# Optimization experiments

Hardware: AMD Instinct MI355X
Metric: run time of the kernel (lower is better)

The kernel has to match this reference:

```python
import jax, jax.numpy as jnp
import numpy as np

N_NODES = 100000
NEG_SLOPE = 0.01


def setup_inputs() -> dict:
    key = jax.random.key(0)
    k1, k2, k3, k4 = jax.random.split(key, 4)
    E = 1600000
    x = jax.random.normal(k1, (N_NODES, 256), dtype=jnp.float32)
    edge_index = jax.random.randint(k2, (2, E), 0, N_NODES, dtype=jnp.int64)
    # Glorot-ish init for GCN linear weights
    W1 = jax.random.normal(k3, (256, 128), dtype=jnp.float32) / np.sqrt(256.0)
    b1 = jnp.zeros((128,), dtype=jnp.float32)
    W2 = jax.random.normal(k4, (128, 64), dtype=jnp.float32) / np.sqrt(128.0)
    b2 = jnp.zeros((64,), dtype=jnp.float32)
    return {"x": x, "edge_index": edge_index, "W1": W1, "b1": b1, "W2": W2, "b2": b2}


def _gcn_norm(edge_index, n_nodes):
    # Add self-loops (PyG GCNConv default), symmetric normalization.
    loops = jnp.arange(n_nodes, dtype=edge_index.dtype)
    src = jnp.concatenate([edge_index[0], loops])
    dst = jnp.concatenate([edge_index[1], loops])
    deg = jax.ops.segment_sum(jnp.ones_like(dst, dtype=jnp.float32), dst,
                              num_segments=n_nodes)
    dinv = jnp.where(deg > 0, 1.0 / jnp.sqrt(deg), 0.0)
    norm = dinv[src] * dinv[dst]  # [E + N]
    return src, dst, norm


def _gcn_conv(h, W, b, src, dst, norm, n_nodes):
    h = h @ W                              # [N, out] linear transform first
    msg = h[src] * norm[:, None]           # gather + edge weighting
    agg = jax.ops.segment_sum(msg, dst, num_segments=n_nodes)  # scatter-add
    return agg + b


def reference(x, edge_index, W1, b1, W2, b2):
    n = x.shape[0]
    src, dst, norm = _gcn_norm(edge_index, n)
    h = _gcn_conv(x, W1, b1, src, dst, norm, n)
    h = jnp.where(h >= 0, h, NEG_SLOPE * h)  # leaky_relu, slope 0.01
    return _gcn_conv(h, W2, b2, src, dst, norm, n)
```

## Files before the change

kernel.cpp:

```cpp
#include <hip/hip_runtime.h>
#include <hip/hip_bf16.h>
#include <stdint.h>

#define GPART 512
#define BSHIFT 9
#define BSIZE 512
#define MAXNB 512

typedef short short8 __attribute__((ext_vector_type(8)));
typedef float f32x4 __attribute__((ext_vector_type(4)));
union U4S8 { uint4 u; short8 s; };

static __device__ __forceinline__ float bflo(uint32_t h){ return __uint_as_float(h << 16); }
static __device__ __forceinline__ float bfhi(uint32_t h){ return __uint_as_float(h & 0xFFFF0000u); }
static __device__ __forceinline__ uint32_t f2bf_bits(float f){
  uint32_t u = __float_as_uint(f);
  return (u + 0x7FFFu + ((u >> 16) & 1u)) >> 16;
}
static __device__ __forceinline__ uint32_t pack2bf(float lo, float hi){
  return f2bf_bits(lo) | (f2bf_bits(hi) << 16);
}

__global__ __launch_bounds__(256) void k_hist(const int* __restrict__ dst, int E, int NB,
    int* __restrict__ gHist){
  __shared__ int lh[MAXNB];
  int blk = blockIdx.x;
  for (int i = threadIdx.x; i < NB; i += 256) lh[i] = 0;
  __syncthreads();
  int chunk = (E + GPART - 1) / GPART;
  int e0 = blk * chunk, e1 = min(E, e0 + chunk);
  for (int e = e0 + threadIdx.x; e < e1; e += 256)
    atomicAdd(&lh[dst[e] >> BSHIFT], 1);
  __syncthreads();
  for (int i = threadIdx.x; i < NB; i += 256) gHist[i * GPART + blk] = lh[i];
}

__global__ __launch_bounds__(64) void k_scanA(int* __restrict__ gHist,
    int* __restrict__ bucketTotal){
  int b = blockIdx.x;
  int lane = threadIdx.x;
  int carry = 0;
  #pragma unroll
  for (int r = 0; r < GPART/64; ++r){
    int v = gHist[b*GPART + r*64 + lane];
    int pref = v;
    #pragma unroll
    for (int off = 1; off < 64; off <<= 1){ int t = __shfl_up(pref, off); if (lane >= off) pref += t; }
    int tot = __shfl(pref, 63);
    gHist[b*GPART + r*64 + lane] = carry + pref - v;
    carry += tot;
  }
  if (lane == 0) bucketTotal[b] = carry;
}

__global__ __launch_bounds__(64) void k_scanB(const int* __restrict__ bucketTotal, int NB,
    int* __restrict__ bucketBase){
  int lane = threadIdx.x;
  int carry = 0;
  for (int r = 0; r*64 < NB; ++r){
    int idx = r*64 + lane;
    int v = (idx < NB) ? bucketTotal[idx] : 0;
    int pref = v;
    #pragma unroll
    for (int off = 1; off < 64; off <<= 1){ int t = __shfl_up(pref, off); if (lane >= off) pref += t; }
    int tot = __shfl(pref, 63);
    if (idx < NB) bucketBase[idx] = carry + pref - v;
    carry += tot;
  }
}

__global__ __launch_bounds__(256) void k_scatter(const int* __restrict__ src,
    const int* __restrict__ dst, int E, int NB,
    const int* __restrict__ gHist, const int* __restrict__ bucketBase,
    uint32_t* __restrict__ edgesP){
  __shared__ int lpos[MAXNB];
  int blk = blockIdx.x;
  for (int i = threadIdx.x; i < NB; i += 256) lpos[i] = 0;
  __syncthreads();
  int chunk = (E + GPART - 1) / GPART;
  int e0 = blk * chunk, e1 = min(E, e0 + chunk);
  for (int e = e0 + threadIdx.x; e < e1; e += 256){
    int s = src[e], d = dst[e];
    int b = d >> BSHIFT;
    int o = atomicAdd(&lpos[b], 1);
    int pos = bucketBase[b] + gHist[b*GPART + blk] + o;
    edgesP[pos] = (uint32_t)s | ((uint32_t)(d & (BSIZE-1)) << 23);
  }
}

__global__ __launch_bounds__(256) void k_csr_p1(const uint32_t* __restrict__ edgesP,
    const int* __restrict__ bucketBase, const int* __restrict__ bucketTotal,
    int n, int* __restrict__ start, int* __restrict__ cnt, float* __restrict__ dinv){
  __shared__ int cnt_l[BSIZE], start_l[BSIZE];
  int b = blockIdx.x;
  int base = bucketBase[b], total = bucketTotal[b];
  int d0 = b << BSHIFT;
  int tid = threadIdx.x;
  for (int i = tid; i < BSIZE; i += 256) cnt_l[i] = 0;
  __syncthreads();
  for (int i = tid; i < total; i += 256)
    atomicAdd(&cnt_l[edgesP[base + i] >> 23], 1);
  __syncthreads();
  if (tid < 64){
    int lane = tid, carry = 0;
    #pragma unroll
    for (int r = 0; r < BSIZE/64; ++r){
      int v = cnt_l[r*64 + lane];
      int pref = v;
      #pragma unroll
      for (int off = 1; off < 64; off <<= 1){ int t = __shfl_up(pref, off); if (lane >= off) pref += t; }
      int tot = __shfl(pref, 63);
      start_l[r*64 + lane] = carry + pref - v;
      carry += tot;
    }
  }
  __syncthreads();
  for (int i = tid; i < BSIZE; i += 256){
    int d = d0 + i;
    if (d < n){
      int c = cnt_l[i];
      cnt[d] = c;
      start[d] = base + start_l[i];
      dinv[d] = rsqrtf((float)(c + 1));
    }
  }
}

__global__ __launch_bounds__(256) void k_csr_p2(const uint32_t* __restrict__ edgesP,
    const int* __restrict__ bucketBase, const int* __restrict__ bucketTotal,
    const int* __restrict__ start, const float* __restrict__ dinv,
    int2* __restrict__ csr){
  __shared__ int fp[BSIZE];
  int b = blockIdx.x;
  int base = bucketBase[b], total = bucketTotal[b];
  int d0 = b << BSHIFT;
  int tid = threadIdx.x;
  for (int i = tid; i < BSIZE; i += 256) fp[i] = 0;
  __syncthreads();
  for (int i = tid; i < total; i += 256){
    uint32_t w = edgesP[base + i];
    int dl = (int)(w >> 23);
    int s = (int)(w & 0x7FFFFFu);
    int p = atomicAdd(&fp[dl], 1);
    float wt = dinv[s] * dinv[d0 + dl];
    csr[start[d0 + dl] + p] = make_int2(s, __float_as_int(wt));
  }
}

__global__ __launch_bounds__(256) void k_packW(const float* __restrict__ W,
    uint4* __restrict__ Wf, int K, int Nc){
  int s = blockIdx.x * 256 + threadIdx.x;
  int total = (K >> 5) * (Nc >> 4) * 64;
  if (s >= total) return;
  int lane = s & 63;
  int frag = s >> 6;
  int NT = Nc >> 4;
  int nt = frag % NT, ks = frag / NT;
  int col = nt*16 + (lane & 15);
  int k0  = ks*32 + (lane >> 4)*8;
  float v[8];
  #pragma unroll
  for (int e = 0; e < 8; ++e) v[e] = W[(size_t)(k0 + e)*Nc + col];
  uint4 u;
  u.x = pack2bf(v[0], v[1]); u.y = pack2bf(v[2], v[3]);
  u.z = pack2bf(v[4], v[5]); u.w = pack2bf(v[6], v[7]);
  Wf[s] = u;
}

__global__ __launch_bounds__(256) void k_gemm1_mfma(const float* __restrict__ X,
    const uint4* __restrict__ W1f, unsigned short* __restrict__ H1, int n){
  int wv = (int)((blockIdx.x * 256u + threadIdx.x) >> 6);
  int lane = threadIdx.x & 63;
  int row0 = wv * 16;
  if (row0 >= n) return;
  int rA = lane & 15, kg = lane >> 4;
  f32x4 acc[8];
  #pragma unroll
  for (int nt = 0; nt < 8; ++nt) acc[nt] = (f32x4){0.f, 0.f, 0.f, 0.f};
  int r0 = min(row0 + rA, n - 1);
  const float* x0 = X + (size_t)r0*256 + kg*8;
  float4 fa = *(const float4*)(x0);
  float4 fb = *(const float4*)(x0 + 4);
  for (int ks = 0; ks < 8; ++ks){
    U4S8 a;
    a.u.x = pack2bf(fa.x, fa.y); a.u.y = pack2bf(fa.z, fa.w);
    a.u.z = pack2bf(fb.x, fb.y); a.u.w = pack2bf(fb.z, fb.w);
    if (ks < 7){
      fa = *(const float4*)(x0 + (ks+1)*32);
      fb = *(const float4*)(x0 + (ks+1)*32 + 4);
    }
    #pragma unroll
    for (int nt = 0; nt < 8; ++nt){
      U4S8 b; b.u = W1f[(ks*8 + nt)*64 + lane];
      acc[nt] = __builtin_amdgcn_mfma_f32_16x16x32_bf16(a.s, b.s, acc[nt], 0, 0, 0);
    }
  }
  #pragma unroll
  for (int r = 0; r < 4; ++r){
    int row = row0 + kg*4 + r;
    if (row < n){
      #pragma unroll
      for (int nt = 0; nt < 8; ++nt)
        H1[(size_t)row*128 + nt*16 + rA] = (unsigned short)f2bf_bits(acc[nt][r]);
    }
  }
}

__global__ __launch_bounds__(256) void k_agg1(const uint4* __restrict__ H1,
    const int2* __restrict__ csr,
    const int* __restrict__ start, const int* __restrict__ cnt,
    const float* __restrict__ dinv, const float* __restrict__ b1,
    uint4* __restrict__ A1, int n){
  int w = (int)((blockIdx.x * blockDim.x + threadIdx.x) >> 6);
  int lane = threadIdx.x & 63;
  if (w >= n) return;
  int g = lane >> 4, li = lane & 15;
  float dw = dinv[w];
  float sw = (g == 0) ? dw * dw : 0.f;
  uint4 hs = H1[(size_t)w*16 + li];
  float acc[8];
  acc[0]=sw*bflo(hs.x); acc[1]=sw*bfhi(hs.x); acc[2]=sw*bflo(hs.y); acc[3]=sw*bfhi(hs.y);
  acc[4]=sw*bflo(hs.z); acc[5]=sw*bfhi(hs.z); acc[6]=sw*bflo(hs.w); acc[7]=sw*bfhi(hs.w);
  int e0 = start[w], deg = cnt[w];
  for (int base = 0; base < deg; base += 64){
    int nin = min(64, deg - base);
    int2 ew = (lane < nin) ? csr[e0 + base + lane] : make_int2(0, 0);
    for (int j = 0; j < nin; j += 8){
      int   sA = __shfl(ew.x, j + g);
      float wA = __uint_as_float((uint32_t)__shfl(ew.y, j + g));
      int   sB = __shfl(ew.x, j + 4 + g);
      float wB = __uint_as_float((uint32_t)__shfl(ew.y, j + 4 + g));
      uint4 hA = H1[(size_t)sA*16 + li];
      uint4 hB = H1[(size_t)sB*16 + li];
      acc[0]=fmaf(wA,bflo(hA.x),acc[0]); acc[1]=fmaf(wA,bfhi(hA.x),acc[1]);
      acc[2]=fmaf(wA,bflo(hA.y),acc[2]); acc[3]=fmaf(wA,bfhi(hA.y),acc[3]);
      acc[4]=fmaf(wA,bflo(hA.z),acc[4]); acc[5]=fmaf(wA,bfhi(hA.z),acc[5]);
      acc[6]=fmaf(wA,bflo(hA.w),acc[6]); acc[7]=fmaf(wA,bfhi(hA.w),acc[7]);
      acc[0]=fmaf(wB,bflo(hB.x),acc[0]); acc[1]=fmaf(wB,bfhi(hB.x),acc[1]);
      acc[2]=fmaf(wB,bflo(hB.y),acc[2]); acc[3]=fmaf(wB,bfhi(hB.y),acc[3]);
      acc[4]=fmaf(wB,bflo(hB.z),acc[4]); acc[5]=fmaf(wB,bfhi(hB.z),acc[5]);
      acc[6]=fmaf(wB,bflo(hB.w),acc[6]); acc[7]=fmaf(wB,bfhi(hB.w),acc[7]);
    }
  }
  #pragma unroll
  for (int e = 0; e < 8; ++e){
    acc[e] += __shfl_xor(acc[e], 16);
    acc[e] += __shfl_xor(acc[e], 32);
  }
  float4 bA = *(const float4*)&b1[li*8];
  float4 bB = *(const float4*)&b1[li*8 + 4];
  acc[0]+=bA.x; acc[1]+=bA.y; acc[2]+=bA.z; acc[3]+=bA.w;
  acc[4]+=bB.x; acc[5]+=bB.y; acc[6]+=bB.z; acc[7]+=bB.w;
  #pragma unroll
  for (int e = 0; e < 8; ++e) acc[e] = (acc[e] >= 0.f) ? acc[e] : 0.01f * acc[e];
  if (g == 0){
    uint4 o;
    o.x = pack2bf(acc[0], acc[1]); o.y = pack2bf(acc[2], acc[3]);
    o.z = pack2bf(acc[4], acc[5]); o.w = pack2bf(acc[6], acc[7]);
    A1[(size_t)w*16 + li] = o;
  }
}

__global__ __launch_bounds__(256) void k_gemm2_mfma(const uint4* __restrict__ A1,
    const uint4* __restrict__ W2f, unsigned short* __restrict__ H2, int n){
  int wv = (int)((blockIdx.x * 256u + threadIdx.x) >> 6);
  int lane = threadIdx.x & 63;
  int row0 = wv * 16;
  if (row0 >= n) return;
  int rA = lane & 15, kg = lane >> 4;
  f32x4 acc[4];
  #pragma unroll
  for (int nt = 0; nt < 4; ++nt) acc[nt] = (f32x4){0.f, 0.f, 0.f, 0.f};
  int r0 = min(row0 + rA, n - 1);
  const uint4* arow = A1 + (size_t)r0*16 + kg;
  uint4 u = arow[0];
  #pragma unroll
  for (int ks = 0; ks < 4; ++ks){
    U4S8 a; a.u = u;
    if (ks < 3) u = arow[(ks+1)*4];
    #pragma unroll
    for (int nt = 0; nt < 4; ++nt){
      U4S8 b; b.u = W2f[(ks*4 + nt)*64 + lane];
      acc[nt] = __builtin_amdgcn_mfma_f32_16x16x32_bf16(a.s, b.s, acc[nt], 0, 0, 0);
    }
  }
  #pragma unroll
  for (int r = 0; r < 4; ++r){
    int row = row0 + kg*4 + r;
    if (row < n){
      #pragma unroll
      for (int nt = 0; nt < 4; ++nt)
        H2[(size_t)row*64 + nt*16 + rA] = (unsigned short)f2bf_bits(acc[nt][r]);
    }
  }
}

__global__ __launch_bounds__(256) void k_agg2(const uint4* __restrict__ H2,
    const int2* __restrict__ csr,
    const int* __restrict__ start, const int* __restrict__ cnt,
    const float* __restrict__ dinv, const float* __restrict__ b2,
    float* __restrict__ out, int n){
  int w = (int)((blockIdx.x * blockDim.x + threadIdx.x) >> 6);
  int lane = threadIdx.x & 63;
  if (w >= n) return;
  int g = lane >> 3, li = lane & 7;
  float dw = dinv[w];
  float sw = (g == 0) ? dw * dw : 0.f;
  uint4 hs = H2[(size_t)w*8 + li];
  float acc[8];
  acc[0]=sw*bflo(hs.x); acc[1]=sw*bfhi(hs.x); acc[2]=sw*bflo(hs.y); acc[3]=sw*bfhi(hs.y);
  acc[4]=sw*bflo(hs.z); acc[5]=sw*bfhi(hs.z); acc[6]=sw*bflo(hs.w); acc[7]=sw*bfhi(hs.w);
  int e0 = start[w], deg = cnt[w];
  for (int base = 0; base < deg; base += 64){
    int nin = min(64, deg - base);
    int2 ew = (lane < nin) ? csr[e0 + base + lane] : make_int2(0, 0);
    for (int j = 0; j < nin; j += 16){
      int   sA = __shfl(ew.x, j + g);
      float wA = __uint_as_float((uint32_t)__shfl(ew.y, j + g));
      int   sB = __shfl(ew.x, j + 8 + g);
      float wB = __uint_as_float((uint32_t)__shfl(ew.y, j + 8 + g));
      uint4 hA = H2[(size_t)sA*8 + li];
      uint4 hB = H2[(size_t)sB*8 + li];
      acc[0]=fmaf(wA,bflo(hA.x),acc[0]); acc[1]=fmaf(wA,bfhi(hA.x),acc[1]);
      acc[2]=fmaf(wA,bflo(hA.y),acc[2]); acc[3]=fmaf(wA,bfhi(hA.y),acc[3]);
      acc[4]=fmaf(wA,bflo(hA.z),acc[4]); acc[5]=fmaf(wA,bfhi(hA.z),acc[5]);
      acc[6]=fmaf(wA,bflo(hA.w),acc[6]); acc[7]=fmaf(wA,bfhi(hA.w),acc[7]);
      acc[0]=fmaf(wB,bflo(hB.x),acc[0]); acc[1]=fmaf(wB,bfhi(hB.x),acc[1]);
      acc[2]=fmaf(wB,bflo(hB.y),acc[2]); acc[3]=fmaf(wB,bfhi(hB.y),acc[3]);
      acc[4]=fmaf(wB,bflo(hB.z),acc[4]); acc[5]=fmaf(wB,bfhi(hB.z),acc[5]);
      acc[6]=fmaf(wB,bflo(hB.w),acc[6]); acc[7]=fmaf(wB,bfhi(hB.w),acc[7]);
    }
  }
  #pragma unroll
  for (int e = 0; e < 8; ++e){
    acc[e] += __shfl_xor(acc[e], 8);
    acc[e] += __shfl_xor(acc[e], 16);
    acc[e] += __shfl_xor(acc[e], 32);
  }
  float4 bA = *(const float4*)&b2[li*8];
  float4 bB = *(const float4*)&b2[li*8 + 4];
  acc[0]+=bA.x; acc[1]+=bA.y; acc[2]+=bA.z; acc[3]+=bA.w;
  acc[4]+=bB.x; acc[5]+=bB.y; acc[6]+=bB.z; acc[7]+=bB.w;
  if (g == 0){
    float4 o0 = make_float4(acc[0], acc[1], acc[2], acc[3]);
    float4 o1 = make_float4(acc[4], acc[5], acc[6], acc[7]);
    *(float4*)&out[(size_t)w*64 + li*8]     = o0;
    *(float4*)&out[(size_t)w*64 + li*8 + 4] = o1;
  }
}

extern "C" void kernel_launch(void* const* d_in, const int* in_sizes, int n_in,
                              void* d_out, int out_size, void* d_ws, size_t ws_size,
                              hipStream_t stream){
  const float* x  = (const float*)d_in[0];
  const int*   ei = (const int*)d_in[1];
  const float* W1 = (const float*)d_in[2];
  const float* b1 = (const float*)d_in[3];
  const float* W2 = (const float*)d_in[4];
  const float* b2 = (const float*)d_in[5];
  float* out = (float*)d_out;

  int N = in_sizes[0] / 256;
  int E = in_sizes[1] / 2;
  int NB = (N + BSIZE - 1) >> BSHIFT;

  char* p = (char*)d_ws;
  uint32_t* H1   = (uint32_t*)p;  p += (size_t)N*64*4;
  uint32_t* A1   = (uint32_t*)p;  p += (size_t)N*64*4;
  uint32_t* H2   = (uint32_t*)p;  p += (size_t)N*32*4;
  uint32_t* edgesP=(uint32_t*)p;  p += (size_t)E*4;
  int2* csr      = (int2*)p;      p += (size_t)E*8;
  int* gHist     = (int*)p;       p += (size_t)NB*GPART*4;
  int* bucketTotal=(int*)p;       p += (size_t)((NB+63)&~63)*4;
  int* bucketBase= (int*)p;       p += (size_t)((NB+63)&~63)*4;
  uint4* W1f     = (uint4*)p;     p += 8*8*64*16;
  uint4* W2f     = (uint4*)p;     p += 4*4*64*16;
  int* start     = (int*)p;       p += (size_t)N*4;
  int* cnt       = (int*)p;       p += (size_t)N*4;
  float* dinv    = (float*)p;     p += (size_t)N*4;

  const int* srcIdx = ei;
  const int* dstIdx = ei + E;

  int nW = (N + 15) / 16;
  int nWaveBlocks = (nW + 3) / 4;

  k_packW<<<(8*8*64 + 255)/256, 256, 0, stream>>>(W1, W1f, 256, 128);
  k_packW<<<(4*4*64 + 255)/256, 256, 0, stream>>>(W2, W2f, 128, 64);
  k_hist<<<GPART, 256, 0, stream>>>(dstIdx, E, NB, gHist);
  k_scanA<<<NB, 64, 0, stream>>>(gHist, bucketTotal);
  k_scanB<<<1, 64, 0, stream>>>(bucketTotal, NB, bucketBase);
  k_scatter<<<GPART, 256, 0, stream>>>(srcIdx, dstIdx, E, NB, gHist, bucketBase, edgesP);
  k_csr_p1<<<NB, 256, 0, stream>>>(edgesP, bucketBase, bucketTotal, N, start, cnt, dinv);
  k_csr_p2<<<NB, 256, 0, stream>>>(edgesP, bucketBase, bucketTotal, start, dinv, csr);
  k_gemm1_mfma<<<nWaveBlocks, 256, 0, stream>>>(x, W1f, (unsigned short*)H1, N);
  k_agg1<<<(N+3)/4, 256, 0, stream>>>((const uint4*)H1, csr, start, cnt, dinv, b1, (uint4*)A1, N);
  k_gemm2_mfma<<<nWaveBlocks, 256, 0, stream>>>((const uint4*)A1, W2f, (unsigned short*)H2, N);
  k_agg2<<<(N+3)/4, 256, 0, stream>>>((const uint4*)H2, csr, start, cnt, dinv, b2, out, N);
}
```

Baseline: 216.4 us.

## Use nontemporal loads/stores for streaming data and prefetch gathers in aggregation

```diff
diff --git a/kernel.cpp b/kernel.cpp
--- a/kernel.cpp
+++ b/kernel.cpp
@@ -9,6 +9,9 @@
 
 typedef short short8 __attribute__((ext_vector_type(8)));
 typedef float f32x4 __attribute__((ext_vector_type(4)));
+typedef uint32_t u32x4 __attribute__((ext_vector_type(4)));
+typedef uint32_t u32x2 __attribute__((ext_vector_type(2)));
+typedef float f32x4v __attribute__((ext_vector_type(4)));
 union U4S8 { uint4 u; short8 s; };
 
 static __device__ __forceinline__ float bflo(uint32_t h){ return __uint_as_float(h << 16); }
@@ -30,7 +33,7 @@
   int chunk = (E + GPART - 1) / GPART;
   int e0 = blk * chunk, e1 = min(E, e0 + chunk);
   for (int e = e0 + threadIdx.x; e < e1; e += 256)
-    atomicAdd(&lh[dst[e] >> BSHIFT], 1);
+    atomicAdd(&lh[__builtin_nontemporal_load(&dst[e]) >> BSHIFT], 1);
   __syncthreads();
   for (int i = threadIdx.x; i < NB; i += 256) gHist[i * GPART + blk] = lh[i];
 }
@@ -80,11 +83,13 @@
   int chunk = (E + GPART - 1) / GPART;
   int e0 = blk * chunk, e1 = min(E, e0 + chunk);
   for (int e = e0 + threadIdx.x; e < e1; e += 256){
-    int s = src[e], d = dst[e];
+    int s = __builtin_nontemporal_load(&src[e]);
+    int d = __builtin_nontemporal_load(&dst[e]);
     int b = d >> BSHIFT;
     int o = atomicAdd(&lpos[b], 1);
     int pos = bucketBase[b] + gHist[b*GPART + blk] + o;
-    edgesP[pos] = (uint32_t)s | ((uint32_t)(d & (BSIZE-1)) << 23);
+    uint32_t v = (uint32_t)s | ((uint32_t)(d & (BSIZE-1)) << 23);
+    __builtin_nontemporal_store(v, &edgesP[pos]);
   }
 }
 
@@ -99,7 +104,7 @@
   for (int i = tid; i < BSIZE; i += 256) cnt_l[i] = 0;
   __syncthreads();
   for (int i = tid; i < total; i += 256)
-    atomicAdd(&cnt_l[edgesP[base + i] >> 23], 1);
+    atomicAdd(&cnt_l[__builtin_nontemporal_load(&edgesP[base + i]) >> 23], 1);
   __syncthreads();
   if (tid < 64){
     int lane = tid, carry = 0;
@@ -138,12 +143,13 @@
   for (int i = tid; i < BSIZE; i += 256) fp[i] = 0;
   __syncthreads();
   for (int i = tid; i < total; i += 256){
-    uint32_t w = edgesP[base + i];
+    uint32_t w = __builtin_nontemporal_load(&edgesP[base + i]);
     int dl = (int)(w >> 23);
     int s = (int)(w & 0x7FFFFFu);
     int p = atomicAdd(&fp[dl], 1);
     float wt = dinv[s] * dinv[d0 + dl];
-    csr[start[d0 + dl] + p] = make_int2(s, __float_as_int(wt));
+    u32x2 v; v.x = (uint32_t)s; v.y = __float_as_uint(wt);
+    __builtin_nontemporal_store(v, (u32x2*)&csr[start[d0 + dl] + p]);
   }
 }
 
@@ -179,15 +185,15 @@
   for (int nt = 0; nt < 8; ++nt) acc[nt] = (f32x4){0.f, 0.f, 0.f, 0.f};
   int r0 = min(row0 + rA, n - 1);
   const float* x0 = X + (size_t)r0*256 + kg*8;
-  float4 fa = *(const float4*)(x0);
-  float4 fb = *(const float4*)(x0 + 4);
+  f32x4v fa = __builtin_nontemporal_load((const f32x4v*)(x0));
+  f32x4v fb = __builtin_nontemporal_load((const f32x4v*)(x0 + 4));
   for (int ks = 0; ks < 8; ++ks){
     U4S8 a;
-    a.u.x = pack2bf(fa.x, fa.y); a.u.y = pack2bf(fa.z, fa.w);
-    a.u.z = pack2bf(fb.x, fb.y); a.u.w = pack2bf(fb.z, fb.w);
+    a.u.x = pack2bf(fa[0], fa[1]); a.u.y = pack2bf(fa[2], fa[3]);
+    a.u.z = pack2bf(fb[0], fb[1]); a.u.w = pack2bf(fb[2], fb[3]);
     if (ks < 7){
-      fa = *(const float4*)(x0 + (ks+1)*32);
-      fb = *(const float4*)(x0 + (ks+1)*32 + 4);
+      fa = __builtin_nontemporal_load((const f32x4v*)(x0 + (ks+1)*32));
+      fb = __builtin_nontemporal_load((const f32x4v*)(x0 + (ks+1)*32 + 4));
     }
     #pragma unroll
     for (int nt = 0; nt < 8; ++nt){
@@ -224,14 +230,29 @@
   int e0 = start[w], deg = cnt[w];
   for (int base = 0; base < deg; base += 64){
     int nin = min(64, deg - base);
-    int2 ew = (lane < nin) ? csr[e0 + base + lane] : make_int2(0, 0);
-    for (int j = 0; j < nin; j += 8){
-      int   sA = __shfl(ew.x, j + g);
-      float wA = __uint_as_float((uint32_t)__shfl(ew.y, j + g));
-      int   sB = __shfl(ew.x, j + 4 + g);
-      float wB = __uint_as_float((uint32_t)__shfl(ew.y, j + 4 + g));
-      uint4 hA = H1[(size_t)sA*16 + li];
-      uint4 hB = H1[(size_t)sB*16 + li];
+    int2 ew;
+    if (lane < nin){
+      u32x2 t = __builtin_nontemporal_load((const u32x2*)&csr[e0 + base + lane]);
+      ew.x = (int)t.x; ew.y = (int)t.y;
+    } else { ew = make_int2(0, 0); }
+    int ninp = (nin + 7) & ~7;
+    int   sA = __shfl(ew.x, g);
+    int   sB = __shfl(ew.x, 4 + g);
+    float wA = __uint_as_float((uint32_t)__shfl(ew.y, g));
+    float wB = __uint_as_float((uint32_t)__shfl(ew.y, 4 + g));
+    uint4 hA = H1[(size_t)sA*16 + li];
+    uint4 hB = H1[(size_t)sB*16 + li];
+    for (int j = 0; j < ninp; j += 8){
+      uint4 hA2, hB2; float wA2 = 0.f, wB2 = 0.f;
+      int jn = j + 8;
+      if (jn < ninp){
+        int sA2 = __shfl(ew.x, jn + g);
+        int sB2 = __shfl(ew.x, jn + 4 + g);
+        wA2 = __uint_as_float((uint32_t)__shfl(ew.y, jn + g));
+        wB2 = __uint_as_float((uint32_t)__shfl(ew.y, jn + 4 + g));
+        hA2 = H1[(size_t)sA2*16 + li];
+        hB2 = H1[(size_t)sB2*16 + li];
+      }
       acc[0]=fmaf(wA,bflo(hA.x),acc[0]); acc[1]=fmaf(wA,bfhi(hA.x),acc[1]);
       acc[2]=fmaf(wA,bflo(hA.y),acc[2]); acc[3]=fmaf(wA,bfhi(hA.y),acc[3]);
       acc[4]=fmaf(wA,bflo(hA.z),acc[4]); acc[5]=fmaf(wA,bfhi(hA.z),acc[5]);
@@ -240,6 +261,7 @@
       acc[2]=fmaf(wB,bflo(hB.y),acc[2]); acc[3]=fmaf(wB,bfhi(hB.y),acc[3]);
       acc[4]=fmaf(wB,bflo(hB.z),acc[4]); acc[5]=fmaf(wB,bfhi(hB.z),acc[5]);
       acc[6]=fmaf(wB,bflo(hB.w),acc[6]); acc[7]=fmaf(wB,bfhi(hB.w),acc[7]);
+      hA = hA2; hB = hB2; wA = wA2; wB = wB2;
     }
   }
   #pragma unroll
@@ -254,10 +276,10 @@
   #pragma unroll
   for (int e = 0; e < 8; ++e) acc[e] = (acc[e] >= 0.f) ? acc[e] : 0.01f * acc[e];
   if (g == 0){
-    uint4 o;
+    u32x4 o;
     o.x = pack2bf(acc[0], acc[1]); o.y = pack2bf(acc[2], acc[3]);
     o.z = pack2bf(acc[4], acc[5]); o.w = pack2bf(acc[6], acc[7]);
-    A1[(size_t)w*16 + li] = o;
+    __builtin_nontemporal_store(o, (u32x4*)&A1[(size_t)w*16 + li]);
   }
 }
 
@@ -272,12 +294,12 @@
   #pragma unroll
   for (int nt = 0; nt < 4; ++nt) acc[nt] = (f32x4){0.f, 0.f, 0.f, 0.f};
   int r0 = min(row0 + rA, n - 1);
-  const uint4* arow = A1 + (size_t)r0*16 + kg;
-  uint4 u = arow[0];
+  const u32x4* arow = (const u32x4*)(A1 + (size_t)r0*16 + kg);
+  u32x4 u = __builtin_nontemporal_load(arow);
   #pragma unroll
   for (int ks = 0; ks < 4; ++ks){
-    U4S8 a; a.u = u;
-    if (ks < 3) u = arow[(ks+1)*4];
+    U4S8 a; a.u.x = u.x; a.u.y = u.y; a.u.z = u.z; a.u.w = u.w;
+    if (ks < 3) u = __builtin_nontemporal_load(arow + (ks+1)*4);
     #pragma unroll
     for (int nt = 0; nt < 4; ++nt){
       U4S8 b; b.u = W2f[(ks*4 + nt)*64 + lane];
@@ -313,14 +335,29 @@
   int e0 = start[w], deg = cnt[w];
   for (int base = 0; base < deg; base += 64){
     int nin = min(64, deg - base);
-    int2 ew = (lane < nin) ? csr[e0 + base + lane] : make_int2(0, 0);
-    for (int j = 0; j < nin; j += 16){
-      int   sA = __shfl(ew.x, j + g);
-      float wA = __uint_as_float((uint32_t)__shfl(ew.y, j + g));
-      int   sB = __shfl(ew.x, j + 8 + g);
-      float wB = __uint_as_float((uint32_t)__shfl(ew.y, j + 8 + g));
-      uint4 hA = H2[(size_t)sA*8 + li];
-      uint4 hB = H2[(size_t)sB*8 + li];
+    int2 ew;
+    if (lane < nin){
+      u32x2 t = __builtin_nontemporal_load((const u32x2*)&csr[e0 + base + lane]);
+      ew.x = (int)t.x; ew.y = (int)t.y;
+    } else { ew = make_int2(0, 0); }
+    int ninp = (nin + 15) & ~15;
+    int   sA = __shfl(ew.x, g);
+    int   sB = __shfl(ew.x, 8 + g);
+    float wA = __uint_as_float((uint32_t)__shfl(ew.y, g));
+    float wB = __uint_as_float((uint32_t)__shfl(ew.y, 8 + g));
+    uint4 hA = H2[(size_t)sA*8 + li];
+    uint4 hB = H2[(size_t)sB*8 + li];
+    for (int j = 0; j < ninp; j += 16){
+      uint4 hA2, hB2; float wA2 = 0.f, wB2 = 0.f;
+      int jn = j + 16;
+      if (jn < ninp){
+        int sA2 = __shfl(ew.x, jn + g);
+        int sB2 = __shfl(ew.x, jn + 8 + g);
+        wA2 = __uint_as_float((uint32_t)__shfl(ew.y, jn + g));
+        wB2 = __uint_as_float((uint32_t)__shfl(ew.y, jn + 8 + g));
+        hA2 = H2[(size_t)sA2*8 + li];
+        hB2 = H2[(size_t)sB2*8 + li];
+      }
       acc[0]=fmaf(wA,bflo(hA.x),acc[0]); acc[1]=fmaf(wA,bfhi(hA.x),acc[1]);
       acc[2]=fmaf(wA,bflo(hA.y),acc[2]); acc[3]=fmaf(wA,bfhi(hA.y),acc[3]);
       acc[4]=fmaf(wA,bflo(hA.z),acc[4]); acc[5]=fmaf(wA,bfhi(hA.z),acc[5]);
@@ -329,6 +366,7 @@
       acc[2]=fmaf(wB,bflo(hB.y),acc[2]); acc[3]=fmaf(wB,bfhi(hB.y),acc[3]);
       acc[4]=fmaf(wB,bflo(hB.z),acc[4]); acc[5]=fmaf(wB,bfhi(hB.z),acc[5]);
       acc[6]=fmaf(wB,bflo(hB.w),acc[6]); acc[7]=fmaf(wB,bfhi(hB.w),acc[7]);
+      hA = hA2; hB = hB2; wA = wA2; wB = wB2;
     }
   }
   #pragma unroll
@@ -342,10 +380,10 @@
   acc[0]+=bA.x; acc[1]+=bA.y; acc[2]+=bA.z; acc[3]+=bA.w;
   acc[4]+=bB.x; acc[5]+=bB.y; acc[6]+=bB.z; acc[7]+=bB.w;
   if (g == 0){
-    float4 o0 = make_float4(acc[0], acc[1], acc[2], acc[3]);
-    float4 o1 = make_float4(acc[4], acc[5], acc[6], acc[7]);
-    *(float4*)&out[(size_t)w*64 + li*8]     = o0;
-    *(float4*)&out[(size_t)w*64 + li*8 + 4] = o1;
+    f32x4v o0; o0[0]=acc[0]; o0[1]=acc[1]; o0[2]=acc[2]; o0[3]=acc[3];
+    f32x4v o1; o1[0]=acc[4]; o1[1]=acc[5]; o1[2]=acc[6]; o1[3]=acc[7];
+    __builtin_nontemporal_store(o0, (f32x4v*)&out[(size_t)w*64 + li*8]);
+    __builtin_nontemporal_store(o1, (f32x4v*)&out[(size_t)w*64 + li*8 + 4]);
   }
 }
 
```

New measurement: 308.7 us. 42.7% more time.

## Split layer-1 aggregation into two column-half passes and software-pipeline gathers

Applied to the files above, without the earlier changes.

```diff
diff --git a/kernel.cpp b/kernel.cpp
--- a/kernel.cpp
+++ b/kernel.cpp
@@ -168,7 +168,8 @@
 }
 
 __global__ __launch_bounds__(256) void k_gemm1_mfma(const float* __restrict__ X,
-    const uint4* __restrict__ W1f, unsigned short* __restrict__ H1, int n){
+    const uint4* __restrict__ W1f, unsigned short* __restrict__ H1a,
+    unsigned short* __restrict__ H1b, int n){
   int wv = (int)((blockIdx.x * 256u + threadIdx.x) >> 6);
   int lane = threadIdx.x & 63;
   int row0 = wv * 16;
@@ -200,68 +201,76 @@
     int row = row0 + kg*4 + r;
     if (row < n){
       #pragma unroll
-      for (int nt = 0; nt < 8; ++nt)
-        H1[(size_t)row*128 + nt*16 + rA] = (unsigned short)f2bf_bits(acc[nt][r]);
-    }
-  }
-}
-
-__global__ __launch_bounds__(256) void k_agg1(const uint4* __restrict__ H1,
+      for (int nt = 0; nt < 4; ++nt)
+        H1a[(size_t)row*64 + nt*16 + rA] = (unsigned short)f2bf_bits(acc[nt][r]);
+      #pragma unroll
+      for (int nt = 4; nt < 8; ++nt)
+        H1b[(size_t)row*64 + (nt-4)*16 + rA] = (unsigned short)f2bf_bits(acc[nt][r]);
+    }
+  }
+}
+
+__global__ __launch_bounds__(256) void k_agg1_pass(const uint2* __restrict__ H1p,
     const int2* __restrict__ csr,
     const int* __restrict__ start, const int* __restrict__ cnt,
-    const float* __restrict__ dinv, const float* __restrict__ b1,
-    uint4* __restrict__ A1, int n){
+    const float* __restrict__ dinv, const float* __restrict__ b1p,
+    uint2* __restrict__ A1p, int n){
   int w = (int)((blockIdx.x * blockDim.x + threadIdx.x) >> 6);
   int lane = threadIdx.x & 63;
   if (w >= n) return;
   int g = lane >> 4, li = lane & 15;
   float dw = dinv[w];
   float sw = (g == 0) ? dw * dw : 0.f;
-  uint4 hs = H1[(size_t)w*16 + li];
-  float acc[8];
+  uint2 hs = H1p[(size_t)w*16 + li];
+  float acc[4];
   acc[0]=sw*bflo(hs.x); acc[1]=sw*bfhi(hs.x); acc[2]=sw*bflo(hs.y); acc[3]=sw*bfhi(hs.y);
-  acc[4]=sw*bflo(hs.z); acc[5]=sw*bfhi(hs.z); acc[6]=sw*bflo(hs.w); acc[7]=sw*bfhi(hs.w);
   int e0 = start[w], deg = cnt[w];
   for (int base = 0; base < deg; base += 64){
     int nin = min(64, deg - base);
     int2 ew = (lane < nin) ? csr[e0 + base + lane] : make_int2(0, 0);
-    for (int j = 0; j < nin; j += 8){
-      int   sA = __shfl(ew.x, j + g);
-      float wA = __uint_as_float((uint32_t)__shfl(ew.y, j + g));
-      int   sB = __shfl(ew.x, j + 4 + g);
-      float wB = __uint_as_float((uint32_t)__shfl(ew.y, j + 4 + g));
-      uint4 hA = H1[(size_t)sA*16 + li];
-      uint4 hB = H1[(size_t)sB*16 + li];
+    int ninp = (nin + 7) & ~7;
+    int   sA = __shfl(ew.x, g);
+    int   sB = __shfl(ew.x, 4 + g);
+    float wA = __uint_as_float((uint32_t)__shfl(ew.y, g));
+    float wB = __uint_as_float((uint32_t)__shfl(ew.y, 4 + g));
+    uint2 hA = H1p[(size_t)sA*16 + li];
+    uint2 hB = H1p[(size_t)sB*16 + li];
+    for (int j = 0; j < ninp; j += 8){
+      uint2 hA2 = hA, hB2 = hB; float wA2 = 0.f, wB2 = 0.f;
+      int jn = j + 8;
+      if (jn < ninp){
+        int sA2 = __shfl(ew.x, jn + g);
+        int sB2 = __shfl(ew.x, jn + 4 + g);
+        wA2 = __uint_as_float((uint32_t)__shfl(ew.y, jn + g));
+        wB2 = __uint_as_float((uint32_t)__shfl(ew.y, jn + 4 + g));
+        hA2 = H1p[(size_t)sA2*16 + li];
+        hB2 = H1p[(size_t)sB2*16 + li];
+      }
       acc[0]=fmaf(wA,bflo(hA.x),acc[0]); acc[1]=fmaf(wA,bfhi(hA.x),acc[1]);
       acc[2]=fmaf(wA,bflo(hA.y),acc[2]); acc[3]=fmaf(wA,bfhi(hA.y),acc[3]);
-      acc[4]=fmaf(wA,bflo(hA.z),acc[4]); acc[5]=fmaf(wA,bfhi(hA.z),acc[5]);
-      acc[6]=fmaf(wA,bflo(hA.w),acc[6]); acc[7]=fmaf(wA,bfhi(hA.w),acc[7]);
       acc[0]=fmaf(wB,bflo(hB.x),acc[0]); acc[1]=fmaf(wB,bfhi(hB.x),acc[1]);
       acc[2]=fmaf(wB,bflo(hB.y),acc[2]); acc[3]=fmaf(wB,bfhi(hB.y),acc[3]);
-      acc[4]=fmaf(wB,bflo(hB.z),acc[4]); acc[5]=fmaf(wB,bfhi(hB.z),acc[5]);
-      acc[6]=fmaf(wB,bflo(hB.w),acc[6]); acc[7]=fmaf(wB,bfhi(hB.w),acc[7]);
-    }
-  }
-  #pragma unroll
-  for (int e = 0; e < 8; ++e){
+      hA = hA2; hB = hB2; wA = wA2; wB = wB2;
+    }
+  }
+  #pragma unroll
+  for (int e = 0; e < 4; ++e){
     acc[e] += __shfl_xor(acc[e], 16);
     acc[e] += __shfl_xor(acc[e], 32);
   }
-  float4 bA = *(const float4*)&b1[li*8];
-  float4 bB = *(const float4*)&b1[li*8 + 4];
-  acc[0]+=bA.x; acc[1]+=bA.y; acc[2]+=bA.z; acc[3]+=bA.w;
-  acc[4]+=bB.x; acc[5]+=bB.y; acc[6]+=bB.z; acc[7]+=bB.w;
-  #pragma unroll
-  for (int e = 0; e < 8; ++e) acc[e] = (acc[e] >= 0.f) ? acc[e] : 0.01f * acc[e];
+  float4 bb = *(const float4*)&b1p[li*4];
+  acc[0]+=bb.x; acc[1]+=bb.y; acc[2]+=bb.z; acc[3]+=bb.w;
+  #pragma unroll
+  for (int e = 0; e < 4; ++e) acc[e] = (acc[e] >= 0.f) ? acc[e] : 0.01f * acc[e];
   if (g == 0){
-    uint4 o;
+    uint2 o;
     o.x = pack2bf(acc[0], acc[1]); o.y = pack2bf(acc[2], acc[3]);
-    o.z = pack2bf(acc[4], acc[5]); o.w = pack2bf(acc[6], acc[7]);
-    A1[(size_t)w*16 + li] = o;
-  }
-}
-
-__global__ __launch_bounds__(256) void k_gemm2_mfma(const uint4* __restrict__ A1,
+    A1p[(size_t)w*16 + li] = o;
+  }
+}
+
+__global__ __launch_bounds__(256) void k_gemm2_mfma(const uint4* __restrict__ A1a,
+    const uint4* __restrict__ A1b,
     const uint4* __restrict__ W2f, unsigned short* __restrict__ H2, int n){
   int wv = (int)((blockIdx.x * 256u + threadIdx.x) >> 6);
   int lane = threadIdx.x & 63;
@@ -272,12 +281,15 @@
   #pragma unroll
   for (int nt = 0; nt < 4; ++nt) acc[nt] = (f32x4){0.f, 0.f, 0.f, 0.f};
   int r0 = min(row0 + rA, n - 1);
-  const uint4* arow = A1 + (size_t)r0*16 + kg;
-  uint4 u = arow[0];
+  const uint4* rowa = A1a + (size_t)r0*8 + kg;
+  const uint4* rowb = A1b + (size_t)r0*8 + kg;
+  uint4 u = rowa[0];
   #pragma unroll
   for (int ks = 0; ks < 4; ++ks){
     U4S8 a; a.u = u;
-    if (ks < 3) u = arow[(ks+1)*4];
+    if (ks == 0) u = rowa[4];
+    else if (ks == 1) u = rowb[0];
+    else if (ks == 2) u = rowb[4];
     #pragma unroll
     for (int nt = 0; nt < 4; ++nt){
       U4S8 b; b.u = W2f[(ks*4 + nt)*64 + lane];
@@ -314,13 +326,24 @@
   for (int base = 0; base < deg; base += 64){
     int nin = min(64, deg - base);
     int2 ew = (lane < nin) ? csr[e0 + base + lane] : make_int2(0, 0);
-    for (int j = 0; j < nin; j += 16){
-      int   sA = __shfl(ew.x, j + g);
-      float wA = __uint_as_float((uint32_t)__shfl(ew.y, j + g));
-      int   sB = __shfl(ew.x, j + 8 + g);
-      float wB = __uint_as_float((uint32_t)__shfl(ew.y, j + 8 + g));
-      uint4 hA = H2[(size_t)sA*8 + li];
-      uint4 hB = H2[(size_t)sB*8 + li];
+    int ninp = (nin + 15) & ~15;
+    int   sA = __shfl(ew.x, g);
+    int   sB = __shfl(ew.x, 8 + g);
+    float wA = __uint_as_float((uint32_t)__shfl(ew.y, g));
+    float wB = __uint_as_float((uint32_t)__shfl(ew.y, 8 + g));
+    uint4 hA = H2[(size_t)sA*8 + li];
+    uint4 hB = H2[(size_t)sB*8 + li];
+    for (int j = 0; j < ninp; j += 16){
+      uint4 hA2 = hA, hB2 = hB; float wA2 = 0.f, wB2 = 0.f;
+      int jn = j + 16;
+      if (jn < ninp){
+        int sA2 = __shfl(ew.x, jn + g);
+        int sB2 = __shfl(ew.x, jn + 8 + g);
+        wA2 = __uint_as_float((uint32_t)__shfl(ew.y, jn + g));
+        wB2 = __uint_as_float((uint32_t)__shfl(ew.y, jn + 8 + g));
+        hA2 = H2[(size_t)sA2*8 + li];
+        hB2 = H2[(size_t)sB2*8 + li];
+      }
       acc[0]=fmaf(wA,bflo(hA.x),acc[0]); acc[1]=fmaf(wA,bfhi(hA.x),acc[1]);
       acc[2]=fmaf(wA,bflo(hA.y),acc[2]); acc[3]=fmaf(wA,bfhi(hA.y),acc[3]);
       acc[4]=fmaf(wA,bflo(hA.z),acc[4]); acc[5]=fmaf(wA,bfhi(hA.z),acc[5]);
@@ -329,6 +352,7 @@
       acc[2]=fmaf(wB,bflo(hB.y),acc[2]); acc[3]=fmaf(wB,bfhi(hB.y),acc[3]);
       acc[4]=fmaf(wB,bflo(hB.z),acc[4]); acc[5]=fmaf(wB,bfhi(hB.z),acc[5]);
       acc[6]=fmaf(wB,bflo(hB.w),acc[6]); acc[7]=fmaf(wB,bfhi(hB.w),acc[7]);
+      hA = hA2; hB = hB2; wA = wA2; wB = wB2;
     }
   }
   #pragma unroll
@@ -365,8 +389,10 @@
   int NB = (N + BSIZE - 1) >> BSHIFT;
 
   char* p = (char*)d_ws;
-  uint32_t* H1   = (uint32_t*)p;  p += (size_t)N*64*4;
-  uint32_t* A1   = (uint32_t*)p;  p += (size_t)N*64*4;
+  uint32_t* H1a  = (uint32_t*)p;  p += (size_t)N*32*4;
+  uint32_t* H1b  = (uint32_t*)p;  p += (size_t)N*32*4;
+  uint32_t* A1a  = (uint32_t*)p;  p += (size_t)N*32*4;
+  uint32_t* A1b  = (uint32_t*)p;  p += (size_t)N*32*4;
   uint32_t* H2   = (uint32_t*)p;  p += (size_t)N*32*4;
   uint32_t* edgesP=(uint32_t*)p;  p += (size_t)E*4;
   int2* csr      = (int2*)p;      p += (size_t)E*8;
@@ -384,6 +410,7 @@
 
   int nW = (N + 15) / 16;
   int nWaveBlocks = (nW + 3) / 4;
+  int nNodeBlocks = (N + 3) / 4;
 
   k_packW<<<(8*8*64 + 255)/256, 256, 0, stream>>>(W1, W1f, 256, 128);
   k_packW<<<(4*4*64 + 255)/256, 256, 0, stream>>>(W2, W2f, 128, 64);
@@ -393,8 +420,13 @@
   k_scatter<<<GPART, 256, 0, stream>>>(srcIdx, dstIdx, E, NB, gHist, bucketBase, edgesP);
   k_csr_p1<<<NB, 256, 0, stream>>>(edgesP, bucketBase, bucketTotal, N, start, cnt, dinv);
   k_csr_p2<<<NB, 256, 0, stream>>>(edgesP, bucketBase, bucketTotal, start, dinv, csr);
-  k_gemm1_mfma<<<nWaveBlocks, 256, 0, stream>>>(x, W1f, (unsigned short*)H1, N);
-  k_agg1<<<(N+3)/4, 256, 0, stream>>>((const uint4*)H1, csr, start, cnt, dinv, b1, (uint4*)A1, N);
-  k_gemm2_mfma<<<nWaveBlocks, 256, 0, stream>>>((const uint4*)A1, W2f, (unsigned short*)H2, N);
-  k_agg2<<<(N+3)/4, 256, 0, stream>>>((const uint4*)H2, csr, start, cnt, dinv, b2, out, N);
-}
+  k_gemm1_mfma<<<nWaveBlocks, 256, 0, stream>>>(x, W1f,
+      (unsigned short*)H1a, (unsigned short*)H1b, N);
+  k_agg1_pass<<<nNodeBlocks, 256, 0, stream>>>((const uint2*)H1a, csr, start, cnt,
+      dinv, b1,      (uint2*)A1a, N);
+  k_agg1_pass<<<nNodeBlocks, 256, 0, stream>>>((const uint2*)H1b, csr, start, cnt,
+      dinv, b1 + 64, (uint2*)A1b, N);
+  k_gemm2_mfma<<<nWaveBlocks, 256, 0, stream>>>((const uint4*)A1a, (const uint4*)A1b,
+      W2f, (unsigned short*)H2, N);
+  k_agg2<<<nNodeBlocks, 256, 0, stream>>>((const uint4*)H2, csr, start, cnt, dinv, b2, out, N);
+}
```

Result: slower. 245.7 us (+13.6%).

## Stage X tiles in LDS via async global_load_lds for first GEMM

Applied to the files above, without the earlier changes.

```diff
diff --git a/kernel.cpp b/kernel.cpp
--- a/kernel.cpp
+++ b/kernel.cpp
@@ -167,41 +167,51 @@
   Wf[s] = u;
 }
 
-__global__ __launch_bounds__(256) void k_gemm1_mfma(const float* __restrict__ X,
+__global__ __launch_bounds__(256) void k_gemm1_lds(const float* __restrict__ X,
     const uint4* __restrict__ W1f, unsigned short* __restrict__ H1, int n){
-  int wv = (int)((blockIdx.x * 256u + threadIdx.x) >> 6);
-  int lane = threadIdx.x & 63;
-  int row0 = wv * 16;
-  if (row0 >= n) return;
+  __shared__ float xs[32][256];
+  int tid = threadIdx.x;
+  int wid = tid >> 6, lane = tid & 63;
+  int row0 = blockIdx.x * 32;
+  #pragma unroll
+  for (int i = 0; i < 8; ++i){
+    int r = wid*8 + i;
+    int gr = min(row0 + r, n - 1);
+    const float* gsrc = X + (size_t)gr*256 + 4*(lane ^ (r & 7));
+    __builtin_amdgcn_global_load_lds(
+        (const __attribute__((address_space(1))) unsigned int*)gsrc,
+        (__attribute__((address_space(3))) unsigned int*)(&xs[r][0]),
+        16, 0, 0);
+  }
+  __syncthreads();
+  int mhalf = wid & 1, nh = wid >> 1;
   int rA = lane & 15, kg = lane >> 4;
-  f32x4 acc[8];
-  #pragma unroll
-  for (int nt = 0; nt < 8; ++nt) acc[nt] = (f32x4){0.f, 0.f, 0.f, 0.f};
-  int r0 = min(row0 + rA, n - 1);
-  const float* x0 = X + (size_t)r0*256 + kg*8;
-  float4 fa = *(const float4*)(x0);
-  float4 fb = *(const float4*)(x0 + 4);
+  int lrow = mhalf*16 + rA;
+  f32x4 acc[4];
+  #pragma unroll
+  for (int nt = 0; nt < 4; ++nt) acc[nt] = (f32x4){0.f, 0.f, 0.f, 0.f};
+  #pragma unroll
   for (int ks = 0; ks < 8; ++ks){
+    int g0 = ks*8 + kg*2;
+    float4 f0 = *(const float4*)&xs[lrow][4*( g0      ^ (rA & 7))];
+    float4 f1 = *(const float4*)&xs[lrow][4*((g0 + 1) ^ (rA & 7))];
     U4S8 a;
-    a.u.x = pack2bf(fa.x, fa.y); a.u.y = pack2bf(fa.z, fa.w);
-    a.u.z = pack2bf(fb.x, fb.y); a.u.w = pack2bf(fb.z, fb.w);
-    if (ks < 7){
-      fa = *(const float4*)(x0 + (ks+1)*32);
-      fb = *(const float4*)(x0 + (ks+1)*32 + 4);
-    }
+    a.u.x = pack2bf(f0.x, f0.y); a.u.y = pack2bf(f0.z, f0.w);
+    a.u.z = pack2bf(f1.x, f1.y); a.u.w = pack2bf(f1.z, f1.w);
     #pragma unroll
-    for (int nt = 0; nt < 8; ++nt){
-      U4S8 b; b.u = W1f[(ks*8 + nt)*64 + lane];
+    for (int nt = 0; nt < 4; ++nt){
+      U4S8 b; b.u = W1f[(ks*8 + nh*4 + nt)*64 + lane];
       acc[nt] = __builtin_amdgcn_mfma_f32_16x16x32_bf16(a.s, b.s, acc[nt], 0, 0, 0);
     }
   }
+  int rowbase = row0 + mhalf*16 + kg*4;
   #pragma unroll
   for (int r = 0; r < 4; ++r){
-    int row = row0 + kg*4 + r;
+    int row = rowbase + r;
     if (row < n){
       #pragma unroll
-      for (int nt = 0; nt < 8; ++nt)
-        H1[(size_t)row*128 + nt*16 + rA] = (unsigned short)f2bf_bits(acc[nt][r]);
+      for (int nt = 0; nt < 4; ++nt)
+        H1[(size_t)row*128 + (nh*4 + nt)*16 + rA] = (unsigned short)f2bf_bits(acc[nt][r]);
     }
   }
 }
@@ -382,8 +392,10 @@
   const int* srcIdx = ei;
   const int* dstIdx = ei + E;
 
-  int nW = (N + 15) / 16;
-  int nWaveBlocks = (nW + 3) / 4;
+  int nG1Blocks = (N + 31) / 32;
+  int nW2 = (N + 15) / 16;
+  int nG2Blocks = (nW2 + 3) / 4;
+  int nNodeBlocks = (N + 3) / 4;
 
   k_packW<<<(8*8*64 + 255)/256, 256, 0, stream>>>(W1, W1f, 256, 128);
   k_packW<<<(4*4*64 + 255)/256, 256, 0, stream>>>(W2, W2f, 128, 64);
@@ -393,8 +405,8 @@
   k_scatter<<<GPART, 256, 0, stream>>>(srcIdx, dstIdx, E, NB, gHist, bucketBase, edgesP);
   k_csr_p1<<<NB, 256, 0, stream>>>(edgesP, bucketBase, bucketTotal, N, start, cnt, dinv);
   k_csr_p2<<<NB, 256, 0, stream>>>(edgesP, bucketBase, bucketTotal, start, dinv, csr);
-  k_gemm1_mfma<<<nWaveBlocks, 256, 0, stream>>>(x, W1f, (unsigned short*)H1, N);
-  k_agg1<<<(N+3)/4, 256, 0, stream>>>((const uint4*)H1, csr, start, cnt, dinv, b1, (uint4*)A1, N);
-  k_gemm2_mfma<<<nWaveBlocks, 256, 0, stream>>>((const uint4*)A1, W2f, (unsigned short*)H2, N);
-  k_agg2<<<(N+3)/4, 256, 0, stream>>>((const uint4*)H2, csr, start, cnt, dinv, b2, out, N);
-}
+  k_gemm1_lds<<<nG1Blocks, 256, 0, stream>>>(x, W1f, (unsigned short*)H1, N);
+  k_agg1<<<nNodeBlocks, 256, 0, stream>>>((const uint4*)H1, csr, start, cnt, dinv, b1, (uint4*)A1, N);
+  k_gemm2_mfma<<<nG2Blocks, 256, 0, stream>>>((const uint4*)A1, W2f, (unsigned short*)H2, N);
+  k_agg2<<<nNodeBlocks, 256, 0, stream>>>((const uint4*)H2, csr, start, cnt, dinv, b2, out, N);
+}
```

Result: no change. 216.3 us (-0.0%).
